# Kernel optimization log

Hardware: AMD Instinct MI355X
Metric: run time of the kernel (lower is better)

Reference implementation:

```python
import jax, jax.numpy as jnp
import numpy as np

B, T, D = 32, 512, 1024
HOP, HID = 8, 350
NEG = jnp.float32(-1e30)  # stand-in for -inf in masked softmax (grad-safe)


def setup_inputs() -> dict:
    key = jax.random.key(0)
    ks = jax.random.split(key, 8)
    s = lambda k, sh, sc: (jax.random.normal(k, sh, jnp.float32) * sc)
    return {
        "input": jax.random.normal(ks[0], (B, T, D), jnp.float32),
        "lg": T,  # unused by the module's forward, kept for signature fidelity
        "W0": s(ks[1], (D, 3 * D), 0.02),
        "b0": jnp.zeros((2 * D,), jnp.float32),
        "W1": s(ks[2], (D, 3 * D), 0.02),
        "b1": jnp.zeros((2 * D,), jnp.float32),
        "ws1": s(ks[3], (HID, D), 0.02),
        "ws2": s(ks[4], (HOP, HID), 0.02),
        "fc_w": s(ks[5], (D, HOP * D), 0.02),
        "fc_b": jnp.zeros((D,), jnp.float32),
    }


def sru_layer(x, W, b):
    # x: [T, B, d]; SRU with use_tanh=True, identity highway (d_in == d_out).
    d = W.shape[1] // 3
    U = jnp.einsum('tbi,ij->tbj', x, W)            # one big GEMM for all gates
    xt = U[..., :d]
    f = jax.nn.sigmoid(U[..., d:2 * d] + b[:d])    # forget gate
    r = jax.nn.sigmoid(U[..., 2 * d:] + b[d:])     # reset/highway gate

    def step(c, u):
        xt_t, f_t = u
        c = f_t * c + (1.0 - f_t) * xt_t
        return c, c

    c0 = jnp.zeros(xt.shape[1:], xt.dtype)
    _, cs = jax.lax.scan(step, c0, (xt, f))        # elementwise gated recurrence
    return r * jnp.tanh(cs) + (1.0 - r) * x


def reference(input, lg, W0, b0, W1, b1, ws1, ws2, fc_w, fc_b):
    # lengths per _process_lengths: T - count of positions where feature-0 == 0
    lengths = T - jnp.sum((input[:, :, 0] == 0).astype(jnp.int32), axis=1)  # [B]

    x = jnp.transpose(input, (1, 0, 2))            # [T, B, D]
    x = sru_layer(x, W0, b0)
    x = sru_layer(x, W1, b1)
    x = jnp.transpose(x, (1, 0, 2))                # [B, T, D]

    # multi-hop self-attention pooling (dropout is identity in eval mode)
    hbar = jnp.tanh(jnp.einsum('btd,hd->bth', x, ws1))   # [B, T, HID]
    alphas = jnp.einsum('bth,kh->bkt', hbar, ws2)        # [B, HOP, T]
    mask = jnp.arange(T)[None, None, :] >= lengths[:, None, None]
    attn = jax.nn.softmax(jnp.where(mask, NEG, alphas), axis=2)  # [B, HOP, T]

    pooled = jnp.einsum('bkt,btd->bkd', attn, x).reshape(input.shape[0], -1)
    out = pooled @ fc_w.T + fc_b                   # [B, D]
    return out, attn
```

## Files before the change

kernel.cpp:

```cpp
#include <hip/hip_runtime.h>
#include <hip/hip_bf16.h>

#define B_ 32
#define T_ 512
#define D_ 1024
#define HOP_ 8
#define HID_ 350
#define NEGV -1e30f
#define CH_ 4

typedef __bf16 v8bf __attribute__((ext_vector_type(8)));
typedef float  v4f  __attribute__((ext_vector_type(4)));

__device__ __forceinline__ float fast_sigmoid(float x) {
    return 1.0f / (1.0f + __expf(-x));
}
__device__ __forceinline__ float fast_tanh(float x) {
    return 1.0f - 2.0f / (__expf(2.0f * x) + 1.0f);
}
__device__ __forceinline__ float bf2f(unsigned short u) {
    unsigned x = ((unsigned)u) << 16;
    float f;
    __builtin_memcpy(&f, &x, 4);
    return f;
}
__device__ __forceinline__ unsigned short f2bf(float v) {
    __hip_bfloat16 h = __float2bfloat16(v);
    unsigned short u;
    __builtin_memcpy(&u, &h, 2);
    return u;
}

__global__ __launch_bounds__(512) void lengths_k(const float* __restrict__ input,
                                                 int* __restrict__ len) {
    int b = blockIdx.x;
    int t = threadIdx.x;
    int z = (input[((size_t)b * T_ + t) * D_] == 0.0f) ? 1 : 0;
    __shared__ int cnt;
    if (t == 0) cnt = 0;
    __syncthreads();
    unsigned long long m = __ballot(z);
    if ((t & 63) == 0) atomicAdd(&cnt, __popcll(m));
    __syncthreads();
    if (t == 0) len[b] = T_ - cnt;
}


__global__ __launch_bounds__(256) void convX_k(const float* __restrict__ in,
                                               unsigned short* __restrict__ out) {
    int i = (blockIdx.x * 256 + threadIdx.x) * 4;
    float4 v = *(const float4*)&in[i];
    out[i + 0] = f2bf(v.x);
    out[i + 1] = f2bf(v.y);
    out[i + 2] = f2bf(v.z);
    out[i + 3] = f2bf(v.w);
}

template <bool NT>
__global__ __launch_bounds__(256) void convW_k(const float* __restrict__ W,
                                               unsigned short* __restrict__ Wp,
                                               int K, int N, int nT, int Nreal) {
    int o = blockIdx.x * 256 + threadIdx.x;
    int tile = o >> 12;
    int within = o & 4095;
    int n_l = within >> 5, k_l = within & 31;
    int kb = tile / nT, nbb = tile % nT;
    int n = nbb * 128 + n_l, k = kb * 32 + k_l;
    float v = 0.f;
    if (NT) {
        if (n < Nreal) v = W[(size_t)n * K + k];
    } else {
        v = W[(size_t)k * N + n];
    }
    Wp[o] = f2bf(v);
}

template <int EPI>
__global__ __launch_bounds__(256) void gemm_mfma(
    const unsigned short* __restrict__ A,
    const unsigned short* __restrict__ Bp,
    void* __restrict__ C,
    int K, int nT, int Nstore) {
    __shared__ __align__(16) char smem[34816];
    unsigned short* As = (unsigned short*)smem;
    unsigned short* Bs = (unsigned short*)(smem + 8192);
    const int tid = threadIdx.x;
    const int lane = tid & 63;
    const int wid = __builtin_amdgcn_readfirstlane(tid >> 6);
    const int wm = wid & 1, wn = wid >> 1;
    const int m0 = blockIdx.y * 128;
    const int n0 = blockIdx.x * 128;
    const int nb = blockIdx.x;
    const int quad = lane >> 4;
    const int l15 = lane & 15;

    v4f acc[4][4];
#pragma unroll
    for (int i = 0; i < 4; ++i)
#pragma unroll
        for (int j = 0; j < 4; ++j) acc[i][j] = (v4f)(0.f);

    const int nKB = K >> 5;
    for (int kb = 0; kb < nKB; ++kb) {
        __syncthreads();
#pragma unroll
        for (int p = 0; p < 2; ++p) {
            int g = p * 256 + wid * 64 + lane;
            const unsigned short* gp = A + (size_t)(m0 + (g >> 2)) * K + kb * 32 + (g & 3) * 8;
            int ldsOff = (p * 256 + wid * 64) * 16;
            __builtin_amdgcn_global_load_lds(
                (const __attribute__((address_space(1))) void*)gp,
                (__attribute__((address_space(3))) void*)((char*)As + ldsOff),
                16, 0, 0);
        }
        const unsigned short* bt = Bp + (size_t)(kb * nT + nb) * (128 * 32);
#pragma unroll
        for (int p = 0; p < 2; ++p) {
            int g = p * 256 + wid * 64 + lane;
            const unsigned short* gp = bt + g * 8;
            int ldsOff = (p * 256 + wid * 64) * 16;
            __builtin_amdgcn_global_load_lds(
                (const __attribute__((address_space(1))) void*)gp,
                (__attribute__((address_space(3))) void*)((char*)Bs + ldsOff),
                16, 0, 0);
        }
        __syncthreads();
        v8bf af[4], bfr[4];
#pragma unroll
        for (int mi = 0; mi < 4; ++mi)
            af[mi] = *(const v8bf*)&As[(wm * 64 + mi * 16 + l15) * 32 + quad * 8];
#pragma unroll
        for (int ni = 0; ni < 4; ++ni)
            bfr[ni] = *(const v8bf*)&Bs[(wn * 64 + ni * 16 + l15) * 32 + quad * 8];
#pragma unroll
        for (int mi = 0; mi < 4; ++mi)
#pragma unroll
            for (int ni = 0; ni < 4; ++ni)
                acc[mi][ni] = __builtin_amdgcn_mfma_f32_16x16x32_bf16(
                    af[mi], bfr[ni], acc[mi][ni], 0, 0, 0);
    }

    if (EPI == 0) {
        __syncthreads();
        unsigned short* Ct = (unsigned short*)smem;
#pragma unroll
        for (int ni = 0; ni < 4; ++ni) {
            int n_l = wn * 64 + ni * 16 + l15;
#pragma unroll
            for (int mi = 0; mi < 4; ++mi) {
                int m_l = wm * 64 + mi * 16 + quad * 4;
                v4f cc = acc[mi][ni];
#pragma unroll
                for (int r = 0; r < 4; ++r)
                    Ct[(m_l + r) * 136 + n_l] = f2bf(cc[r]);
            }
        }
        __syncthreads();
        int row = tid >> 1;
        int colH = (tid & 1) << 6;
        unsigned short* gdst = (unsigned short*)C + (size_t)(m0 + row) * 3072 + n0 + colH;
        const unsigned short* lsrc = Ct + row * 136 + colH;
#pragma unroll
        for (int i = 0; i < 8; ++i) {
            uint4 v = *(const uint4*)(lsrc + i * 8);
            *(uint4*)(gdst + i * 8) = v;
        }
    } else {
        const int baseM = m0 + wm * 64;
        const int baseN = n0 + wn * 64;
        float* Cf = (float*)C;
#pragma unroll
        for (int ni = 0; ni < 4; ++ni) {
            int j = baseN + ni * 16 + l15;
            if (j < Nstore) {
#pragma unroll
                for (int mi = 0; mi < 4; ++mi) {
                    int m = baseM + mi * 16 + quad * 4;
                    v4f c = acc[mi][ni];
#pragma unroll
                    for (int r = 0; r < 4; ++r)
                        Cf[(size_t)(m + r) * Nstore + j] = fast_tanh(c[r]);
                }
            }
        }
    }
}

__global__ __launch_bounds__(512) void sru_scan_seg(
    const unsigned short* __restrict__ Up,
    const float* __restrict__ bias,
    const unsigned short* __restrict__ xres,
    unsigned short* __restrict__ xout) {
    int b = blockIdx.x >> 5;
    int d0 = (blockIdx.x & 31) << 5;
    int dl = threadIdx.x & 31;
    int s = threadIdx.x >> 5;
    int d = d0 + dl;
    float bf = bias[d], br = bias[D_ + d];
    const unsigned short* Ub = Up + (size_t)b * T_ * 3072 + d;
    const int t0 = s * 32;

    float xt[32], fv[32];
    float Aa = 1.f, Bv = 0.f;
#pragma unroll
    for (int j = 0; j < 32; ++j) {
        const unsigned short* u = Ub + (size_t)(t0 + j) * 3072;
        xt[j] = bf2f(u[0]);
        float f = fast_sigmoid(bf2f(u[1024]) + bf);
        fv[j] = f;
        Aa *= f;
        Bv = f * Bv + (1.f - f) * xt[j];
    }
    __shared__ float Asm[16][32], Bsm[16][32], cinS[16][32];
    Asm[s][dl] = Aa;
    Bsm[s][dl] = Bv;
    __syncthreads();
    if (threadIdx.x < 32) {
        float c = 0.f;
#pragma unroll
        for (int ss = 0; ss < 16; ++ss) {
            cinS[ss][threadIdx.x] = c;
            c = Asm[ss][threadIdx.x] * c + Bsm[ss][threadIdx.x];
        }
    }
    __syncthreads();
    float c = cinS[s][dl];
    const unsigned short* xr = xres + (size_t)b * T_ * D_ + d;
    unsigned short* ob = xout + (size_t)b * T_ * D_ + d;
#pragma unroll
    for (int j = 0; j < 32; ++j) {
        int t = t0 + j;
        float r = fast_sigmoid(bf2f(Ub[(size_t)t * 3072 + 2048]) + br);
        c = fv[j] * c + (1.f - fv[j]) * xt[j];
        float xv = bf2f(xr[(size_t)t * D_]);
        float o = r * fast_tanh(c) + (1.f - r) * xv;
        ob[(size_t)t * D_] = f2bf(o);
    }
}


template <bool BT, bool DO_TANH>
__global__ __launch_bounds__(256) void gemm64(const float* __restrict__ A,
                                              const float* __restrict__ Bm,
                                              float* __restrict__ C,
                                              int M, int N, int K) {
    __shared__ float Asm[16][64];
    __shared__ float Bsm[16][64];
    const int tid = threadIdx.x;
    const int tx = tid & 15;
    const int ty = tid >> 4;
    const int m0 = blockIdx.y * 64;
    const int n0 = blockIdx.x * 64;
    float acc[4][4] = {};
    const int ar = tid >> 2;
    const int ac = (tid & 3) << 2;

    for (int k0 = 0; k0 < K; k0 += 16) {
        {
            float4 v = *(const float4*)&A[(size_t)(m0 + ar) * K + k0 + ac];
            Asm[ac + 0][ar] = v.x; Asm[ac + 1][ar] = v.y;
            Asm[ac + 2][ar] = v.z; Asm[ac + 3][ar] = v.w;
        }
        if (!BT) {
            int kk = tid >> 4;
            int c4 = (tid & 15) << 2;
            float4 v = *(const float4*)&Bm[(size_t)(k0 + kk) * N + n0 + c4];
            Bsm[kk][c4 + 0] = v.x; Bsm[kk][c4 + 1] = v.y;
            Bsm[kk][c4 + 2] = v.z; Bsm[kk][c4 + 3] = v.w;
        } else {
            int nn = tid >> 2;
            int kk = (tid & 3) << 2;
            int row = n0 + nn;
            if (row < N) {
                float4 v = *(const float4*)&Bm[(size_t)row * K + k0 + kk];
                Bsm[kk + 0][nn] = v.x; Bsm[kk + 1][nn] = v.y;
                Bsm[kk + 2][nn] = v.z; Bsm[kk + 3][nn] = v.w;
            } else {
                Bsm[kk + 0][nn] = 0.f; Bsm[kk + 1][nn] = 0.f;
                Bsm[kk + 2][nn] = 0.f; Bsm[kk + 3][nn] = 0.f;
            }
        }
        __syncthreads();
#pragma unroll
        for (int kk = 0; kk < 16; ++kk) {
            float4 a = *(const float4*)&Asm[kk][ty << 2];
            float4 b = *(const float4*)&Bsm[kk][tx << 2];
            float am[4] = {a.x, a.y, a.z, a.w};
            float bm[4] = {b.x, b.y, b.z, b.w};
#pragma unroll
            for (int i = 0; i < 4; ++i)
#pragma unroll
                for (int j = 0; j < 4; ++j)
                    acc[i][j] += am[i] * bm[j];
        }
        __syncthreads();
    }
#pragma unroll
    for (int i = 0; i < 4; ++i) {
        int row = m0 + (ty << 2) + i;
#pragma unroll
        for (int j = 0; j < 4; ++j) {
            int col = n0 + (tx << 2) + j;
            if (col < N) {
                float v = acc[i][j];
                if (DO_TANH) v = fast_tanh(v);
                C[(size_t)row * N + col] = v;
            }
        }
    }
}

__global__ __launch_bounds__(256) void sru_scan(const float* __restrict__ U,
                                                const float* __restrict__ bias,
                                                const float* __restrict__ xin,
                                                float* __restrict__ xout) {
    int idx = blockIdx.x * 256 + threadIdx.x;
    int b = idx >> 10;
    int d = idx & (D_ - 1);
    float bfv = bias[d], br = bias[D_ + d];
    float c = 0.0f;
    const float* Ub = U + (size_t)b * T_ * (3 * D_);
    const float* xb = xin + (size_t)b * T_ * D_;
    float* ob = xout + (size_t)b * T_ * D_;
    for (int t = 0; t < T_; t += 8) {
        float ux[8], uf[8], ur[8], xv[8];
#pragma unroll
        for (int j = 0; j < 8; ++j) {
            const float* u = Ub + (size_t)(t + j) * (3 * D_);
            ux[j] = u[d];
            uf[j] = u[D_ + d];
            ur[j] = u[2 * D_ + d];
            xv[j] = xb[(size_t)(t + j) * D_ + d];
        }
#pragma unroll
        for (int j = 0; j < 8; ++j) {
            float f = fast_sigmoid(uf[j] + bfv);
            float r = fast_sigmoid(ur[j] + br);
            c = f * c + (1.0f - f) * ux[j];
            ob[(size_t)(t + j) * D_ + d] = r * fast_tanh(c) + (1.0f - r) * xv[j];
        }
    }
}


__global__ __launch_bounds__(256) void alphas_k(const float* __restrict__ hbar,
                                                const float* __restrict__ ws2,
                                                float* __restrict__ alph) {
    __shared__ float w[HOP_][352];
    for (int i = threadIdx.x; i < HOP_ * HID_; i += 256)
        w[i / HID_][i % HID_] = ws2[i];
    __syncthreads();
    int bt = blockIdx.x * 256 + threadIdx.x;
    const float* hr = hbar + (size_t)bt * HID_;
    float acc[HOP_] = {};
    for (int h = 0; h < HID_; ++h) {
        float hv = hr[h];
#pragma unroll
        for (int k = 0; k < HOP_; ++k) acc[k] += w[k][h] * hv;
    }
    float* ar = alph + (size_t)bt * HOP_;
#pragma unroll
    for (int k = 0; k < HOP_; ++k) ar[k] = acc[k];
}

__global__ __launch_bounds__(256) void softmax_k(const float* __restrict__ alph,
                                                 const int* __restrict__ len,
                                                 float* __restrict__ attn) {
    int b = blockIdx.x >> 3, k = blockIdx.x & 7;
    int L = len[b];
    int t0 = threadIdx.x, t1 = threadIdx.x + 256;
    float v0 = (t0 >= L) ? NEGV : alph[((size_t)b * T_ + t0) * HOP_ + k];
    float v1 = (t1 >= L) ? NEGV : alph[((size_t)b * T_ + t1) * HOP_ + k];
    __shared__ float redm[4];
    __shared__ float reds[4];
    float m = fmaxf(v0, v1);
#pragma unroll
    for (int off = 32; off; off >>= 1) m = fmaxf(m, __shfl_xor(m, off));
    if ((threadIdx.x & 63) == 0) redm[threadIdx.x >> 6] = m;
    __syncthreads();
    m = fmaxf(fmaxf(redm[0], redm[1]), fmaxf(redm[2], redm[3]));
    float e0 = __expf(v0 - m), e1 = __expf(v1 - m);
    float s = e0 + e1;
#pragma unroll
    for (int off = 32; off; off >>= 1) s += __shfl_xor(s, off);
    if ((threadIdx.x & 63) == 0) reds[threadIdx.x >> 6] = s;
    __syncthreads();
    s = reds[0] + reds[1] + reds[2] + reds[3];
    float inv = 1.0f / s;
    float* ar = attn + ((size_t)b * HOP_ + k) * T_;
    ar[t0] = e0 * inv;
    ar[t1] = e1 * inv;
}

__global__ __launch_bounds__(256) void pooled_bf_k(const float* __restrict__ attn,
                                                   const unsigned short* __restrict__ x2b,
                                                   float* __restrict__ pooled) {
    __shared__ float at[HOP_][T_];
    int b = blockIdx.x >> 2;
    int d0 = (blockIdx.x & 3) * 256;
    for (int i = threadIdx.x; i < HOP_ * T_; i += 256)
        at[i >> 9][i & (T_ - 1)] = attn[(size_t)b * HOP_ * T_ + i];
    __syncthreads();
    int d = d0 + threadIdx.x;
    float acc[HOP_] = {};
    const unsigned short* xb = x2b + (size_t)b * T_ * D_ + d;
    for (int t = 0; t < T_; ++t) {
        float xv = bf2f(xb[(size_t)t * D_]);
#pragma unroll
        for (int k = 0; k < HOP_; ++k) acc[k] += at[k][t] * xv;
    }
#pragma unroll
    for (int k = 0; k < HOP_; ++k)
        pooled[((size_t)b * HOP_ + k) * D_ + d] = acc[k];
}

__global__ __launch_bounds__(256) void pooled_k(const float* __restrict__ attn,
                                                const float* __restrict__ x2,
                                                float* __restrict__ pooled) {
    __shared__ float at[HOP_][T_];
    int b = blockIdx.x >> 2;
    int d0 = (blockIdx.x & 3) * 256;
    for (int i = threadIdx.x; i < HOP_ * T_; i += 256)
        at[i >> 9][i & (T_ - 1)] = attn[(size_t)b * HOP_ * T_ + i];
    __syncthreads();
    int d = d0 + threadIdx.x;
    float acc[HOP_] = {};
    const float* xb = x2 + (size_t)b * T_ * D_ + d;
    for (int t = 0; t < T_; ++t) {
        float xv = xb[(size_t)t * D_];
#pragma unroll
        for (int k = 0; k < HOP_; ++k) acc[k] += at[k][t] * xv;
    }
#pragma unroll
    for (int k = 0; k < HOP_; ++k)
        pooled[((size_t)b * HOP_ + k) * D_ + d] = acc[k];
}

__global__ __launch_bounds__(256) void fc_k(const float* __restrict__ pooled,
                                            const float* __restrict__ fcw,
                                            const float* __restrict__ fcb,
                                            float* __restrict__ out) {
    __shared__ float w[8][1028];
    int j0 = blockIdx.x * 8;
    int b = threadIdx.x >> 3, jj = threadIdx.x & 7;
    float acc = 0.0f;
    for (int p0 = 0; p0 < HOP_ * D_; p0 += 1024) {
        __syncthreads();
        for (int i = threadIdx.x * 4; i < 8 * 1024; i += 256 * 4) {
            int r = i >> 10, c = i & 1023;
            *(float4*)&w[r][c] = *(const float4*)&fcw[(size_t)(j0 + r) * (HOP_ * D_) + p0 + c];
        }
        __syncthreads();
        const float* pr = pooled + (size_t)b * (HOP_ * D_) + p0;
#pragma unroll 4
        for (int i = 0; i < 1024; i += 4) {
            float4 wv = *(const float4*)&w[jj][i];
            float4 pv = *(const float4*)&pr[i];
            acc += wv.x * pv.x + wv.y * pv.y + wv.z * pv.z + wv.w * pv.w;
        }
    }
    out[(size_t)b * D_ + j0 + jj] = acc + fcb[j0 + jj];
}

extern "C" void kernel_launch(void* const* d_in, const int* in_sizes, int n_in,
                              void* d_out, int out_size, void* d_ws, size_t ws_size,
                              hipStream_t stream) {
    const float* input = (const float*)d_in[0];
    const float* W0   = (const float*)d_in[2];
    const float* b0   = (const float*)d_in[3];
    const float* W1   = (const float*)d_in[4];
    const float* b1   = (const float*)d_in[5];
    const float* ws1  = (const float*)d_in[6];
    const float* ws2  = (const float*)d_in[7];
    const float* fc_w = (const float*)d_in[8];
    const float* fc_b = (const float*)d_in[9];

    float* out  = (float*)d_out;
    float* attn = out + (size_t)B_ * D_;
    (void)in_sizes; (void)n_in; (void)out_size;

    const int M = B_ * T_;
    char* ws = (char*)d_ws;

    const size_t NEED_A = 181141632ull;
    const size_t NEED_B = 80478336ull;
    const size_t NEED_FB = 100663424ull;

    if (ws_size >= NEED_B) {
        const int CHv = (ws_size >= NEED_A) ? 32 : 8;
        const int Mc = CHv * T_;
        const size_t szU = (size_t)CHv * 512 * 3072 * 2;
        const size_t szX = (size_t)CHv * 512 * 1024 * 2;
        unsigned short* Uc   = (unsigned short*)ws;
        unsigned short* xbc  = (unsigned short*)(ws + szU);
        unsigned short* x2b  = (unsigned short*)(ws + szU + szX);
        unsigned short* W0p  = (unsigned short*)(ws + szU + szX + 33554432);
        unsigned short* W1p  = W0p + 3145728;
        unsigned short* ws1p = W1p + 3145728;
        int*            len  = (int*)(ws1p + 393216);
        float* hbar   = (float*)ws;
        float* alph   = (float*)(ws + 22937600);
        float* pooled = (float*)(ws + 23461888);

        lengths_k<<<B_, 512, 0, stream>>>(input, len);
        convW_k<false><<<(D_ * 3 * D_) / 256, 256, 0, stream>>>(W0, W0p, D_, 3 * D_, 24, 3 * D_);
        convW_k<false><<<(D_ * 3 * D_) / 256, 256, 0, stream>>>(W1, W1p, D_, 3 * D_, 24, 3 * D_);
        convW_k<true><<<(D_ * 384) / 256, 256, 0, stream>>>(ws1, ws1p, D_, 384, 3, HID_);

        for (int c0 = 0; c0 < B_; c0 += CHv) {
            const float* inC = input + (size_t)c0 * T_ * D_;
            convX_k<<<(Mc * D_ / 4) / 256, 256, 0, stream>>>(inC, xbc);
            gemm_mfma<0><<<dim3(24, Mc / 128), 256, 0, stream>>>(xbc, W0p, Uc, D_, 24, 0);
            sru_scan_seg<<<CHv * 32, 512, 0, stream>>>(Uc, b0, xbc, xbc);
            gemm_mfma<0><<<dim3(24, Mc / 128), 256, 0, stream>>>(xbc, W1p, Uc, D_, 24, 0);
            sru_scan_seg<<<CHv * 32, 512, 0, stream>>>(
                Uc, b1, xbc, x2b + (size_t)c0 * T_ * D_);
        }

        gemm_mfma<1><<<dim3(3, M / 128), 256, 0, stream>>>(x2b, ws1p, hbar, D_, 3, HID_);

        alphas_k<<<M / 256, 256, 0, stream>>>(hbar, ws2, alph);
        softmax_k<<<B_ * HOP_, 256, 0, stream>>>(alph, len, attn);
        pooled_bf_k<<<B_ * 4, 256, 0, stream>>>(attn, x2b, pooled);
        fc_k<<<D_ / 8, 256, 0, stream>>>(pooled, fc_w, fc_b, out);
        return;
    }

    if (ws_size < NEED_FB) return;

    float* U    = (float*)ws;
    float* x1c  = (float*)(ws + 25165824);
    float* x2   = (float*)(ws + 33554432);
    int*   len  = (int*)(ws + 100663296);
    float* hbar   = (float*)ws;
    float* alph   = (float*)(ws + 22937600);
    float* pooled = (float*)(ws + 23461888);

    lengths_k<<<B_, 512, 0, stream>>>(input, len);

    const int Mc = CH_ * T_;
    for (int c0 = 0; c0 < B_; c0 += CH_) {
        const float* inC = input + (size_t)c0 * T_ * D_;
        float* x2C = x2 + (size_t)c0 * T_ * D_;
        gemm64<false, false><<<dim3(3 * D_ / 64, Mc / 64), 256, 0, stream>>>(
            inC, W0, U, Mc, 3 * D_, D_);
        sru_scan<<<CH_ * D_ / 256, 256, 0, stream>>>(U, b0, inC, x1c);
        gemm64<false, false><<<dim3(3 * D_ / 64, Mc / 64), 256, 0, stream>>>(
            x1c, W1, U, Mc, 3 * D_, D_);
        sru_scan<<<CH_ * D_ / 256, 256, 0, stream>>>(U, b1, x1c, x2C);
    }

    gemm64<true, true><<<dim3((HID_ + 63) / 64, M / 64), 256, 0, stream>>>(
        x2, ws1, hbar, M, HID_, D_);
    alphas_k<<<M / 256, 256, 0, stream>>>(hbar, ws2, alph);
    softmax_k<<<B_ * HOP_, 256, 0, stream>>>(alph, len, attn);
    pooled_k<<<B_ * 4, 256, 0, stream>>>(attn, x2, pooled);
    fc_k<<<D_ / 8, 256, 0, stream>>>(pooled, fc_w, fc_b, out);
}
```

Baseline: 828.8 us.

## Tile activation and gate buffers into 64-wide feature chunks for contiguous scan access

```diff
diff --git a/kernel.cpp b/kernel.cpp
--- a/kernel.cpp
+++ b/kernel.cpp
@@ -9,6 +9,7 @@
 #define NEGV -1e30f
 #define CH_ 4
 
+
 typedef __bf16 v8bf __attribute__((ext_vector_type(8)));
 typedef float  v4f  __attribute__((ext_vector_type(4)));
 
@@ -49,11 +50,14 @@
 __global__ __launch_bounds__(256) void convX_k(const float* __restrict__ in,
                                                unsigned short* __restrict__ out) {
     int i = (blockIdx.x * 256 + threadIdx.x) * 4;
+    int m = i >> 10, d = i & 1023;
     float4 v = *(const float4*)&in[i];
-    out[i + 0] = f2bf(v.x);
-    out[i + 1] = f2bf(v.y);
-    out[i + 2] = f2bf(v.z);
-    out[i + 3] = f2bf(v.w);
+    int bb = m >> 9, t = m & 511;
+    unsigned short* o = out + (size_t)bb * 524288 + (size_t)(d >> 6) * 32768 + t * 64 + (d & 63);
+    o[0] = f2bf(v.x);
+    o[1] = f2bf(v.y);
+    o[2] = f2bf(v.z);
+    o[3] = f2bf(v.w);
 }
 
 template <bool NT>
@@ -103,10 +107,14 @@
     const int nKB = K >> 5;
     for (int kb = 0; kb < nKB; ++kb) {
         __syncthreads();
+#pragma
 #pragma unroll
         for (int p = 0; p < 2; ++p) {
             int g = p * 256 + wid * 64 + lane;
-            const unsigned short* gp = A + (size_t)(m0 + (g >> 2)) * K + kb * 32 + (g & 3) * 8;
+            int m = m0 + (g >> 2);
+            int k = kb * 32 + (g & 3) * 8;
+            const unsigned short* gp = A + (size_t)(m >> 9) * 524288 +
+                                       (size_t)(k >> 6) * 32768 + (m & 511) * 64 + (k & 63);
             int ldsOff = (p * 256 + wid * 64) * 16;
             __builtin_amdgcn_global_load_lds(
                 (const __attribute__((address_space(1))) void*)gp,
@@ -158,7 +166,12 @@
         __syncthreads();
         int row = tid >> 1;
         int colH = (tid & 1) << 6;
-        unsigned short* gdst = (unsigned short*)C + (size_t)(m0 + row) * 3072 + n0 + colH;
+        int m = m0 + row;
+        int n = n0 + colH;
+        int p = n >> 10;
+        int dcs = (n & 1023) >> 6;
+        unsigned short* gdst = (unsigned short*)C + (size_t)(m >> 9) * 1572864 +
+                               (size_t)dcs * 98304 + (size_t)(m & 511) * 192 + p * 64;
         const unsigned short* lsrc = Ct + row * 136 + colH;
 #pragma unroll
         for (int i = 0; i < 8; ++i) {
@@ -191,50 +204,50 @@
     const float* __restrict__ bias,
     const unsigned short* __restrict__ xres,
     unsigned short* __restrict__ xout) {
-    int b = blockIdx.x >> 5;
-    int d0 = (blockIdx.x & 31) << 5;
-    int dl = threadIdx.x & 31;
-    int s = threadIdx.x >> 5;
-    int d = d0 + dl;
+    int b = blockIdx.x >> 4;
+    int dc = blockIdx.x & 15;
+    int dl = threadIdx.x & 63;
+    int s = threadIdx.x >> 6;
+    int d = dc * 64 + dl;
     float bf = bias[d], br = bias[D_ + d];
-    const unsigned short* Ub = Up + (size_t)b * T_ * 3072 + d;
-    const int t0 = s * 32;
-
-    float xt[32], fv[32];
+    const unsigned short* Ub = Up + (size_t)b * 1572864 + (size_t)dc * 98304 + dl;
+    const int t0 = s * 64;
+
+    float xt[64], fv[64];
     float Aa = 1.f, Bv = 0.f;
 #pragma unroll
-    for (int j = 0; j < 32; ++j) {
-        const unsigned short* u = Ub + (size_t)(t0 + j) * 3072;
+    for (int j = 0; j < 64; ++j) {
+        const unsigned short* u = Ub + (size_t)(t0 + j) * 192;
         xt[j] = bf2f(u[0]);
-        float f = fast_sigmoid(bf2f(u[1024]) + bf);
+        float f = fast_sigmoid(bf2f(u[64]) + bf);
         fv[j] = f;
         Aa *= f;
         Bv = f * Bv + (1.f - f) * xt[j];
     }
-    __shared__ float Asm[16][32], Bsm[16][32], cinS[16][32];
+    __shared__ float Asm[8][64], Bsm[8][64], cinS[8][64];
     Asm[s][dl] = Aa;
     Bsm[s][dl] = Bv;
     __syncthreads();
-    if (threadIdx.x < 32) {
+    if (threadIdx.x < 64) {
         float c = 0.f;
 #pragma unroll
-        for (int ss = 0; ss < 16; ++ss) {
+        for (int ss = 0; ss < 8; ++ss) {
             cinS[ss][threadIdx.x] = c;
             c = Asm[ss][threadIdx.x] * c + Bsm[ss][threadIdx.x];
         }
     }
     __syncthreads();
     float c = cinS[s][dl];
-    const unsigned short* xr = xres + (size_t)b * T_ * D_ + d;
-    unsigned short* ob = xout + (size_t)b * T_ * D_ + d;
-#pragma unroll
-    for (int j = 0; j < 32; ++j) {
+    const unsigned short* xr = xres + (size_t)b * 524288 + (size_t)dc * 32768 + dl;
+    unsigned short* ob = xout + (size_t)b * 524288 + (size_t)dc * 32768 + dl;
+#pragma unroll
+    for (int j = 0; j < 64; ++j) {
         int t = t0 + j;
-        float r = fast_sigmoid(bf2f(Ub[(size_t)t * 3072 + 2048]) + br);
+        float r = fast_sigmoid(bf2f(Ub[(size_t)t * 192 + 128]) + br);
         c = fv[j] * c + (1.f - fv[j]) * xt[j];
-        float xv = bf2f(xr[(size_t)t * D_]);
+        float xv = bf2f(xr[(size_t)t * 64]);
         float o = r * fast_tanh(c) + (1.f - r) * xv;
-        ob[(size_t)t * D_] = f2bf(o);
+        ob[(size_t)t * 64] = f2bf(o);
     }
 }
 
@@ -403,9 +416,9 @@
     __syncthreads();
     int d = d0 + threadIdx.x;
     float acc[HOP_] = {};
-    const unsigned short* xb = x2b + (size_t)b * T_ * D_ + d;
+    const unsigned short* xb = x2b + (size_t)b * 524288 + (size_t)(d >> 6) * 32768 + (d & 63);
     for (int t = 0; t < T_; ++t) {
-        float xv = bf2f(xb[(size_t)t * D_]);
+        float xv = bf2f(xb[(size_t)t * 64]);
 #pragma unroll
         for (int k = 0; k < HOP_; ++k) acc[k] += at[k][t] * xv;
     }
@@ -511,10 +524,10 @@
             const float* inC = input + (size_t)c0 * T_ * D_;
             convX_k<<<(Mc * D_ / 4) / 256, 256, 0, stream>>>(inC, xbc);
             gemm_mfma<0><<<dim3(24, Mc / 128), 256, 0, stream>>>(xbc, W0p, Uc, D_, 24, 0);
-            sru_scan_seg<<<CHv * 32, 512, 0, stream>>>(Uc, b0, xbc, xbc);
+            sru_scan_seg<<<CHv * 16, 512, 0, stream>>>(Uc, b0, xbc, xbc);
             gemm_mfma<0><<<dim3(24, Mc / 128), 256, 0, stream>>>(xbc, W1p, Uc, D_, 24, 0);
-            sru_scan_seg<<<CHv * 32, 512, 0, stream>>>(
-                Uc, b1, xbc, x2b + (size_t)c0 * T_ * D_);
+            sru_scan_seg<<<CHv * 16, 512, 0, stream>>>(
+                Uc, b1, xbc, x2b + (size_t)c0 * 524288);
         }
 
         gemm_mfma<1><<<dim3(3, M / 128), 256, 0, stream>>>(x2b, ws1p, hbar, D_, 3, HID_);
```

Result: slower. 891.2 us (+7.5%).
